# Kernel optimization log

Hardware: AMD Instinct MI355X
Metric: run time of the kernel (lower is better)

## Reference

```python
import jax, jax.numpy as jnp
import numpy as np

N = 50000      # batch_node_num (unique nodes)
E = 800000     # number of edges (avg degree 16)
IN = 128       # in_dim
OUT = 128      # out_dim
B = 10000      # query nodes


def setup_inputs() -> dict:
    key = jax.random.key(0)
    k = jax.random.split(key, 8)
    edges = jax.random.randint(k[0], (E, 2), 0, N, dtype=jnp.int64)
    node_idx = jax.random.randint(k[1], (B,), 0, N, dtype=jnp.int64)
    local_features = jax.random.normal(k[2], (N, IN), dtype=jnp.float32)
    W1 = jax.random.normal(k[3], (IN, OUT), dtype=jnp.float32) * (1.0 / np.sqrt(IN))
    b1 = jnp.zeros((OUT,), dtype=jnp.float32)
    W2 = jax.random.normal(k[4], (OUT, OUT), dtype=jnp.float32) * (1.0 / np.sqrt(OUT))
    b2 = jnp.zeros((OUT,), dtype=jnp.float32)
    return {"edges": edges, "node_idx": node_idx, "local_features": local_features,
            "W1": W1, "b1": b1, "W2": W2, "b2": b2, "ind": 2}


def reference(edges, node_idx, local_features, W1, b1, W2, b2, ind):
    mask = jnp.array([1.0, 1.0, 0.0, 0.0], dtype=jnp.float32)
    # Linear -> Tanh -> Linear (the out_linear_layer MLP)
    h = jnp.tanh(local_features @ W1 + b1) @ W2 + b2          # [N, OUT]
    src, dst = edges[:, 0], edges[:, 1]
    # self-loop edges get weight mask[ind], others weight 1
    values = jnp.where(src == dst, mask[ind], jnp.float32(1.0))  # [E]
    # spmm(matrix, ones) == per-row degree (weighted)
    row_sum = jax.ops.segment_sum(values, src, num_segments=N)   # [N]
    row_sum = jnp.where(row_sum == 0, jnp.float32(1.0), row_sum)
    # spmm(matrix, new_embeddings): gather dst embeddings, scatter-add to src
    results = jax.ops.segment_sum(values[:, None] * h[dst], src, num_segments=N)  # [N, OUT]
    output_emb = results / row_sum[:, None]
    return output_emb[node_idx]
```

## Files before the change

### kernel.cpp

```cpp
#include <hip/hip_runtime.h>

#define IN_DIM 128
#define CAP 128
#define LDT 136
#define SCAT_BLOCKS 384

typedef short v8s __attribute__((ext_vector_type(8)));
typedef float v4f __attribute__((ext_vector_type(4)));

__device__ inline unsigned short f2bf(float f) {
    unsigned int u = __float_as_uint(f);
    u += 0x7FFFu + ((u >> 16) & 1u);
    return (unsigned short)(u >> 16);
}
__device__ inline float bf2f(unsigned short h) {
    return __uint_as_float((unsigned int)h << 16);
}

__global__ __launch_bounds__(256) void prep(
    const float* __restrict__ W1, const float* __restrict__ W2,
    unsigned short* __restrict__ Wt1, unsigned short* __restrict__ Wt2,
    const int* __restrict__ node_idx, int* __restrict__ flag, int B,
    int* __restrict__ cursor, int N, int nbF)
{
    int bid = blockIdx.x;
    if (bid < 128) {
        int i = bid * 256 + threadIdx.x;
        int m = i >> 14, rem = i & 16383;
        int n = rem >> 7, k = rem & 127;
        float wv = (m ? W2 : W1)[k * 128 + n];
        int idx = n * 128 + (((k >> 3) ^ (n & 15)) << 3) + (k & 7);
        (m ? Wt2 : Wt1)[idx] = f2bf(wv);
    } else if (bid < 128 + nbF) {
        int i = (bid - 128) * 256 + threadIdx.x;
        if (i < B) flag[node_idx[i]] = 1;
    } else {
        int i = (bid - 128 - nbF) * 256 + threadIdx.x;
        if (i < N) cursor[i] = 0;
    }
}

__global__ __launch_bounds__(256, 2) void mlp_fill(
    const float* __restrict__ X,
    const unsigned short* __restrict__ Wt1, const unsigned short* __restrict__ Wt2,
    const float* __restrict__ b1, const float* __restrict__ b2,
    unsigned short* __restrict__ Hb, int nrows,
    const int* __restrict__ edges, const int* __restrict__ flag,
    const int* __restrict__ indp, int* __restrict__ cursor,
    unsigned short* __restrict__ col, int E, int mlpBlocks)
{
    const int bid = blockIdx.x;

    if (bid >= mlpBlocks) {
        const int keepSelf = (*indp < 2) ? 1 : 0;
        const int stride = SCAT_BLOCKS * 256;
        for (int e = (bid - mlpBlocks) * 256 + threadIdx.x; e < E; e += stride) {
            int2 ed = ((const int2*)edges)[e];
            if ((ed.x != ed.y || keepSelf) && flag[ed.x] == 1) {
                int p = atomicAdd(&cursor[ed.x], 1);
                if (p < CAP)
                    col[(size_t)ed.x * CAP + p] = (unsigned short)ed.y;
            }
        }
        return;
    }

    __shared__ uint4 Wl4[2048];
    __shared__ unsigned short Ts[4 * 32 * LDT];
    const unsigned short* Wls = (const unsigned short*)Wl4;
    const int t    = threadIdx.x;
    const int w    = t >> 6;
    const int lane = t & 63;
    const int l15  = lane & 15;
    const int quad = lane >> 4;
    const int R0   = bid * 128;
    const int wrow = w * 32;
    unsigned short* Tw = &Ts[w * 32 * LDT];

    int gr0 = R0 + wrow + l15;        gr0 = gr0 < nrows ? gr0 : nrows - 1;
    int gr1 = R0 + wrow + 16 + l15;   gr1 = gr1 < nrows ? gr1 : nrows - 1;
    const float* xrow[2] = { &X[(size_t)gr0 * 128 + quad * 8],
                             &X[(size_t)gr1 * 128 + quad * 8] };

#pragma unroll
    for (int j = 0; j < 8; ++j)
        Wl4[j * 256 + t] = ((const uint4*)Wt1)[j * 256 + t];

    v4f acc[2][8];
#pragma unroll
    for (int rt = 0; rt < 2; ++rt)
#pragma unroll
        for (int ct = 0; ct < 8; ++ct)
            acc[rt][ct] = (v4f){0.f, 0.f, 0.f, 0.f};

    __syncthreads();

#pragma unroll
    for (int kk = 0; kk < 4; ++kk) {
        v8s Bf[8];
#pragma unroll
        for (int ct = 0; ct < 8; ++ct)
            Bf[ct] = *(const v8s*)
                &Wls[(ct * 16 + l15) * 128 + (((kk * 4 + quad) ^ l15) * 8)];
        v8s Ar[2];
#pragma unroll
        for (int rt = 0; rt < 2; ++rt) {
            const float* xp = xrow[rt] + kk * 32;
            float4 x0 = *(const float4*)xp;
            float4 x1 = *(const float4*)(xp + 4);
            v8s av;
            av[0] = (short)f2bf(x0.x); av[1] = (short)f2bf(x0.y);
            av[2] = (short)f2bf(x0.z); av[3] = (short)f2bf(x0.w);
            av[4] = (short)f2bf(x1.x); av[5] = (short)f2bf(x1.y);
            av[6] = (short)f2bf(x1.z); av[7] = (short)f2bf(x1.w);
            Ar[rt] = av;
        }
#pragma unroll
        for (int ct = 0; ct < 8; ++ct)
#pragma unroll
            for (int rt = 0; rt < 2; ++rt)
                acc[rt][ct] = __builtin_amdgcn_mfma_f32_16x16x32_bf16(
                    Ar[rt], Bf[ct], acc[rt][ct], 0, 0, 0);
    }
#pragma unroll
    for (int ct = 0; ct < 8; ++ct) {
        float bias = b1[ct * 16 + l15];
#pragma unroll
        for (int rt = 0; rt < 2; ++rt) {
#pragma unroll
            for (int r = 0; r < 4; ++r)
                Tw[(rt * 16 + quad * 4 + r) * LDT + ct * 16 + l15] =
                    f2bf(tanhf(acc[rt][ct][r] + bias));
            acc[rt][ct] = (v4f){0.f, 0.f, 0.f, 0.f};
        }
    }

    __syncthreads();
#pragma unroll
    for (int j = 0; j < 8; ++j)
        Wl4[j * 256 + t] = ((const uint4*)Wt2)[j * 256 + t];
    __syncthreads();

#pragma unroll
    for (int kk = 0; kk < 4; ++kk) {
        v8s Bf[8];
#pragma unroll
        for (int ct = 0; ct < 8; ++ct)
            Bf[ct] = *(const v8s*)
                &Wls[(ct * 16 + l15) * 128 + (((kk * 4 + quad) ^ l15) * 8)];
        v8s Ar[2];
#pragma unroll
        for (int rt = 0; rt < 2; ++rt)
            Ar[rt] = *(const v8s*)
                &Tw[(rt * 16 + l15) * LDT + kk * 32 + quad * 8];
#pragma unroll
        for (int ct = 0; ct < 8; ++ct)
#pragma unroll
            for (int rt = 0; rt < 2; ++rt)
                acc[rt][ct] = __builtin_amdgcn_mfma_f32_16x16x32_bf16(
                    Ar[rt], Bf[ct], acc[rt][ct], 0, 0, 0);
    }
    asm volatile("s_waitcnt lgkmcnt(0)" ::: "memory");
#pragma unroll
    for (int ct = 0; ct < 8; ++ct) {
        float bias = b2[ct * 16 + l15];
#pragma unroll
        for (int rt = 0; rt < 2; ++rt)
#pragma unroll
            for (int r = 0; r < 4; ++r)
                Tw[(rt * 16 + quad * 4 + r) * LDT + ct * 16 + l15] =
                    f2bf(acc[rt][ct][r] + bias);
    }
    asm volatile("s_waitcnt lgkmcnt(0)" ::: "memory");
#pragma unroll
    for (int i = 0; i < 8; ++i) {
        int lr = i * 4 + quad;
        int c  = l15;
        uint4 v = *(const uint4*)&Tw[lr * LDT + c * 8];
        int grow = R0 + wrow + lr;
        if (grow < nrows)
            *(uint4*)&Hb[(size_t)grow * 128 + c * 8] = v;
    }
}

__global__ __launch_bounds__(256) void aggregate_out(
    const int* __restrict__ node_idx, const int* __restrict__ cursor,
    const unsigned short* __restrict__ col, const unsigned short* __restrict__ Hb,
    float* __restrict__ out, int B)
{
    int b = (int)((blockIdx.x * blockDim.x + threadIdx.x) >> 6);
    if (b >= B) return;
    int lane = threadIdx.x & 63;
    int v = node_idx[b];
    int deg = cursor[v];
    deg = deg < CAP ? deg : CAP;
    const unsigned short* cp = &col[(size_t)v * CAP];
    int myc = (lane < deg) ? (int)cp[lane] : 0;
    int dmax = deg < 64 ? deg : 64;
    float ax = 0.f, ay = 0.f, bx = 0.f, by = 0.f;
    int i = 0;
    for (; i + 1 < dmax; i += 2) {
        int d0 = __shfl(myc, i, 64);
        int d1 = __shfl(myc, i + 1, 64);
        unsigned int u0 = *(const unsigned int*)&Hb[(size_t)d0 * 128 + lane * 2];
        unsigned int u1 = *(const unsigned int*)&Hb[(size_t)d1 * 128 + lane * 2];
        ax += bf2f((unsigned short)(u0 & 0xFFFFu));
        ay += bf2f((unsigned short)(u0 >> 16));
        bx += bf2f((unsigned short)(u1 & 0xFFFFu));
        by += bf2f((unsigned short)(u1 >> 16));
    }
    if (i < dmax) {
        int d0 = __shfl(myc, i, 64);
        unsigned int u0 = *(const unsigned int*)&Hb[(size_t)d0 * 128 + lane * 2];
        ax += bf2f((unsigned short)(u0 & 0xFFFFu));
        ay += bf2f((unsigned short)(u0 >> 16));
    }
    for (int j = 64; j < deg; ++j) {
        int d0 = cp[j];
        unsigned int u0 = *(const unsigned int*)&Hb[(size_t)d0 * 128 + lane * 2];
        ax += bf2f((unsigned short)(u0 & 0xFFFFu));
        ay += bf2f((unsigned short)(u0 >> 16));
    }
    float den = (deg > 0) ? (float)deg : 1.0f;
    *(float2*)&out[(size_t)b * 128 + lane * 2] =
        make_float2((ax + bx) / den, (ay + by) / den);
}

extern "C" void kernel_launch(void* const* d_in, const int* in_sizes, int n_in,
                              void* d_out, int out_size, void* d_ws, size_t ws_size,
                              hipStream_t stream)
{
    const int*   edges    = (const int*)d_in[0];
    const int*   node_idx = (const int*)d_in[1];
    const float* X        = (const float*)d_in[2];
    const float* W1       = (const float*)d_in[3];
    const float* b1       = (const float*)d_in[4];
    const float* W2       = (const float*)d_in[5];
    const float* b2       = (const float*)d_in[6];
    const int*   indp     = (const int*)d_in[7];

    const int E = in_sizes[0] / 2;
    const int B = in_sizes[1];
    const int N = in_sizes[2] / IN_DIM;
    const int mlpBlocks = (N + 127) / 128;
    const int nbF = (B + 255) / 256;
    const int nbC = (N + 255) / 256;

    char* ws = (char*)d_ws;
    size_t off = 0;
    int* cursor = (int*)(ws + off); off += (size_t)N * 4;
    int* flag   = (int*)(ws + off); off += (size_t)N * 4;
    off = (off + 15) & ~(size_t)15;
    unsigned short* Hb  = (unsigned short*)(ws + off); off += (size_t)N * IN_DIM * 2;
    unsigned short* col = (unsigned short*)(ws + off); off += (size_t)N * CAP * 2;
    unsigned short* Wt1 = (unsigned short*)(ws + off); off += 16384 * 2;
    unsigned short* Wt2 = (unsigned short*)(ws + off); off += 16384 * 2;

    hipLaunchKernelGGL(prep, dim3(128 + nbF + nbC), dim3(256), 0, stream,
                       W1, W2, Wt1, Wt2, node_idx, flag, B, cursor, N, nbF);
    hipLaunchKernelGGL(mlp_fill, dim3(mlpBlocks + SCAT_BLOCKS), dim3(256),
                       0, stream, X, Wt1, Wt2, b1, b2, Hb, N,
                       edges, flag, indp, cursor, col, E, mlpBlocks);
    hipLaunchKernelGGL(aggregate_out, dim3((B * 64 + 255) / 256), dim3(256), 0,
                       stream, node_idx, cursor, col, Hb, (float*)d_out, B);
}
```

Baseline: 122.8 us.

## Stream weights in two K-halves through half-size LDS to raise occupancy

The weight matrices are re-laid out as two K-halves of 64, and the MLP kernel keeps only one half (16KB) in LDS at a time. The second half is prefetched into registers and swapped in mid-loop behind extra barriers. Launch bounds go from 2 to 3 blocks per CU, using the freed LDS to raise occupancy. The cost is more __syncthreads, register pressure from the prefetch buffers, and a narrower 8-way XOR swizzle that may raise LDS bank conflicts.

```diff
diff --git a/kernel.cpp b/kernel.cpp
--- a/kernel.cpp
+++ b/kernel.cpp
@@ -29,7 +29,8 @@
         int m = i >> 14, rem = i & 16383;
         int n = rem >> 7, k = rem & 127;
         float wv = (m ? W2 : W1)[k * 128 + n];
-        int idx = n * 128 + (((k >> 3) ^ (n & 15)) << 3) + (k & 7);
+        int half = k >> 6, ch = (k >> 3) & 7, k0 = k & 7;
+        int idx = half * 8192 + n * 64 + ((ch ^ (n & 7)) << 3) + k0;
         (m ? Wt2 : Wt1)[idx] = f2bf(wv);
     } else if (bid < 128 + nbF) {
         int i = (bid - 128) * 256 + threadIdx.x;
@@ -40,7 +41,7 @@
     }
 }
 
-__global__ __launch_bounds__(256, 2) void mlp_fill(
+__global__ __launch_bounds__(256, 3) void mlp_fill(
     const float* __restrict__ X,
     const unsigned short* __restrict__ Wt1, const unsigned short* __restrict__ Wt2,
     const float* __restrict__ b1, const float* __restrict__ b2,
@@ -65,7 +66,7 @@
         return;
     }
 
-    __shared__ uint4 Wl4[2048];
+    __shared__ uint4 Wl4[1024];
     __shared__ unsigned short Ts[4 * 32 * LDT];
     const unsigned short* Wls = (const unsigned short*)Wl4;
     const int t    = threadIdx.x;
@@ -82,9 +83,10 @@
     const float* xrow[2] = { &X[(size_t)gr0 * 128 + quad * 8],
                              &X[(size_t)gr1 * 128 + quad * 8] };
 
-#pragma unroll
-    for (int j = 0; j < 8; ++j)
-        Wl4[j * 256 + t] = ((const uint4*)Wt1)[j * 256 + t];
+    uint4 wreg[4];
+#pragma unroll
+    for (int j = 0; j < 4; ++j)
+        wreg[j] = ((const uint4*)Wt1)[j * 256 + t];
 
     v4f acc[2][8];
 #pragma unroll
@@ -93,15 +95,27 @@
         for (int ct = 0; ct < 8; ++ct)
             acc[rt][ct] = (v4f){0.f, 0.f, 0.f, 0.f};
 
+#pragma unroll
+    for (int j = 0; j < 4; ++j) Wl4[j * 256 + t] = wreg[j];
     __syncthreads();
+#pragma unroll
+    for (int j = 0; j < 4; ++j)
+        wreg[j] = ((const uint4*)(Wt1 + 8192))[j * 256 + t];
 
 #pragma unroll
     for (int kk = 0; kk < 4; ++kk) {
+        if (kk == 2) {
+            __syncthreads();
+#pragma unroll
+            for (int j = 0; j < 4; ++j) Wl4[j * 256 + t] = wreg[j];
+            __syncthreads();
+        }
+        const int kk2 = kk & 1;
         v8s Bf[8];
 #pragma unroll
         for (int ct = 0; ct < 8; ++ct)
             Bf[ct] = *(const v8s*)
-                &Wls[(ct * 16 + l15) * 128 + (((kk * 4 + quad) ^ l15) * 8)];
+                &Wls[(ct * 16 + l15) * 64 + ((((kk2 * 4 + quad)) ^ (l15 & 7)) << 3)];
         v8s Ar[2];
 #pragma unroll
         for (int rt = 0; rt < 2; ++rt) {
@@ -134,20 +148,31 @@
             acc[rt][ct] = (v4f){0.f, 0.f, 0.f, 0.f};
         }
     }
-
+#pragma unroll
+    for (int j = 0; j < 4; ++j)
+        wreg[j] = ((const uint4*)Wt2)[j * 256 + t];
     __syncthreads();
 #pragma unroll
-    for (int j = 0; j < 8; ++j)
-        Wl4[j * 256 + t] = ((const uint4*)Wt2)[j * 256 + t];
+    for (int j = 0; j < 4; ++j) Wl4[j * 256 + t] = wreg[j];
     __syncthreads();
+#pragma unroll
+    for (int j = 0; j < 4; ++j)
+        wreg[j] = ((const uint4*)(Wt2 + 8192))[j * 256 + t];
 
 #pragma unroll
     for (int kk = 0; kk < 4; ++kk) {
+        if (kk == 2) {
+            __syncthreads();
+#pragma unroll
+            for (int j = 0; j < 4; ++j) Wl4[j * 256 + t] = wreg[j];
+            __syncthreads();
+        }
+        const int kk2 = kk & 1;
         v8s Bf[8];
 #pragma unroll
         for (int ct = 0; ct < 8; ++ct)
             Bf[ct] = *(const v8s*)
-                &Wls[(ct * 16 + l15) * 128 + (((kk * 4 + quad) ^ l15) * 8)];
+                &Wls[(ct * 16 + l15) * 64 + ((((kk2 * 4 + quad)) ^ (l15 & 7)) << 3)];
         v8s Ar[2];
 #pragma unroll
         for (int rt = 0; rt < 2; ++rt)
```

Result: slower. 128.4 us (+4.5%).
